# Performance work log

Hardware: AMD Instinct MI355X
Metric: run time of the kernel (lower is better)

## Reference

```python
import jax, jax.numpy as jnp
import numpy as np

EPS = 1e-05
BOUNDARY = 1.0 - EPS
LAMBDA_REP = 1.0


def poincare_dist_matrix(z):
    # z: [B, D]. Pairwise Poincare distance, same math as PoincareDistance.forward:
    #   squnorm = clamp(|u|^2, 0, boundary); sqdist = |u - v|^2 (unclamped)
    #   x = 2*sqdist/((1-squnorm)*(1-sqvnorm)) + 1; d = log(x + sqrt(x^2 - 1))
    sq = jnp.sum(z * z, axis=-1)                      # [B] raw squared norms
    squ = jnp.clip(sq, 0.0, BOUNDARY)                 # clamped norms (as in torch)
    # |u-v|^2 via norms + gram matrix (avoids materializing [B,B,D])
    sqdist = jnp.maximum(sq[:, None] + sq[None, :] - 2.0 * (z @ z.T), 0.0)  # [B,B]
    alpha = 1.0 - squ
    x = sqdist / (alpha[:, None] * alpha[None, :]) * 2.0 + 1.0
    # safe sqrt: diagonal has x==1 exactly; clamp mirrors torch backward's clamp(min=eps)
    t = jnp.sqrt(jnp.maximum(x * x - 1.0, EPS * EPS))
    return jnp.log(x + t)


def setup_inputs() -> dict:
    key = jax.random.key(0)
    k1, k2, k3, k4 = jax.random.split(key, 4)
    N, B, D = 8192, 4096, 16
    z = jax.random.normal(k1, (B, D), dtype=jnp.float32)
    # place embeddings strictly inside the Poincare ball (norm < 0.7)
    z = 0.7 * z / (1.0 + jnp.linalg.norm(z, axis=-1, keepdims=True))
    w_vals = jax.random.uniform(k2, (N, N), dtype=jnp.float32)
    keep = jax.random.uniform(k3, (N, N)) < 0.05
    W = jnp.where(keep, w_vals, 0.0)
    indices = jax.random.randint(k4, (B,), 0, N)
    return {"z": z, "W": W, "indices": indices}


def reference(z, W, indices):
    B = z.shape[0]
    W_batch = W[indices][:, indices]                  # [B,B] gathered weights
    eye = jnp.eye(B, dtype=bool)
    W_batch = jnp.where(eye, 0.0, W_batch)
    D_low = poincare_dist_matrix(z)                   # [B,B]
    non_neighbors = jnp.where(eye, 0.0, (W_batch == 0.0).astype(z.dtype))
    loss_attract = jnp.sum(W_batch * D_low) / (jnp.sum(W_batch) + 1e-08)
    loss_repel = jnp.sum(non_neighbors * jnp.exp(-D_low)) / (jnp.sum(non_neighbors) + 1e-08)
    return loss_attract + LAMBDA_REP * loss_repel
```

## Files before the change

### kernel.cpp

```cpp
#include <hip/hip_runtime.h>
#include <math.h>

#define TI 32
#define BLOCK 512
#define DIM 16
#define JC 256

typedef short bf16x8 __attribute__((ext_vector_type(8)));
typedef float f32x16 __attribute__((ext_vector_type(16)));

static __device__ __forceinline__ short f2bf(float f) {
    unsigned u = __builtin_bit_cast(unsigned, f);
    unsigned r = (u + 0x7FFFu + ((u >> 16) & 1u)) >> 16;
    return (short)r;
}

__global__ __launch_bounds__(1024) void sort_kernel(
    const int* __restrict__ idx, int B, int N,
    int* __restrict__ perm, int* __restrict__ skey)
{
    extern __shared__ int hist[];
    __shared__ int wsum[16];
    const int tid = threadIdx.x;
    const int lane = tid & 63, wid = tid >> 6;
    for (int b = tid; b < N; b += 1024) hist[b] = 0;
    __syncthreads();
    for (int j = tid; j < B; j += 1024) atomicAdd(&hist[idx[j]], 1);
    __syncthreads();
    const int PB = (N + 1023) >> 10;
    int local[8];
    int sum = 0;
    #pragma unroll
    for (int q = 0; q < 8; ++q) {
        if (q < PB) {
            int b = tid * PB + q;
            local[q] = sum;
            if (b < N) sum += hist[b];
        }
    }
    int v = sum;
    for (int off = 1; off < 64; off <<= 1) {
        int u = __shfl_up(v, off);
        if (lane >= off) v += u;
    }
    if (lane == 63) wsum[wid] = v;
    __syncthreads();
    if (tid < 16) {
        int t = wsum[tid];
        for (int off = 1; off < 16; off <<= 1) {
            int u = __shfl_up(t, off);
            if (lane >= off) t += u;
        }
        wsum[tid] = t;
    }
    __syncthreads();
    int base = (wid == 0) ? 0 : wsum[wid - 1];
    int excl = base + v - sum;
    #pragma unroll
    for (int q = 0; q < 8; ++q) {
        if (q < PB) {
            int b = tid * PB + q;
            if (b < N) hist[b] = excl + local[q];
        }
    }
    __syncthreads();
    for (int j = tid; j < B; j += 1024) {
        int k = idx[j];
        int pos = atomicAdd(&hist[k], 1);
        perm[pos] = j;
        skey[pos] = k;
    }
}

__global__ __launch_bounds__(256) void prep_kernel(
    const float* __restrict__ z, const int* __restrict__ perm, int B,
    float* __restrict__ zs, float* __restrict__ sqs, float* __restrict__ ras)
{
    int r = blockIdx.x * 256 + threadIdx.x;
    if (r >= B) return;
    int p = perm[r];
    const float4* src = reinterpret_cast<const float4*>(z + (size_t)p * DIM);
    float4* dst = reinterpret_cast<float4*>(zs + (size_t)r * DIM);
    float s = 0.f;
    #pragma unroll
    for (int q = 0; q < 4; ++q) {
        float4 v = src[q];
        dst[q] = v;
        s = fmaf(v.x, v.x, s); s = fmaf(v.y, v.y, s);
        s = fmaf(v.z, v.z, s); s = fmaf(v.w, v.w, s);
    }
    sqs[r] = s;
    float sc = fminf(fmaxf(s, 0.f), 0.99999f);
    ras[r] = 1.0f / (1.0f - sc);
}

__global__ __launch_bounds__(BLOCK, 4) void pair_kernel(
    const float* __restrict__ W, const int* __restrict__ skey,
    const float* __restrict__ zs, const float* __restrict__ sqs,
    const float* __restrict__ ras,
    int B, int N, double* __restrict__ partial)
{
    __shared__ double red[BLOCK / 64][4];

    const int tid  = threadIdx.x;
    const int wv   = tid >> 6;
    const int lane = tid & 63;
    const int half = lane >> 5;
    const int sub  = lane & 31;
    const int i0   = blockIdx.x * TI;
    const int jr0  = blockIdx.y * JC;

    const int irow  = i0 + sub;
    const int jrank = jr0 + wv * 32 + sub;
    const int kj    = skey[jrank];

    float wg[16];
    #pragma unroll
    for (int r = 0; r < 16; ++r) {
        const int rowm = (r & 3) + 8 * (r >> 2) + 4 * half;
        const int skr  = skey[i0 + rowm];
        wg[r] = W[(size_t)skr * (size_t)N + (size_t)kj];
    }

    const float ui = ras[irow],  vi = sqs[irow]  * ui;
    const float uj = ras[jrank], vj = sqs[jrank] * uj;
    bf16x8 a1, b1, a2, b2;
    {
        const float4* zp = reinterpret_cast<const float4*>(zs + (size_t)irow * DIM + 8 * half);
        float4 p0 = zp[0], p1 = zp[1];
        float s = 2.0f * ui;
        a1[0]=f2bf(s*p0.x); a1[1]=f2bf(s*p0.y); a1[2]=f2bf(s*p0.z); a1[3]=f2bf(s*p0.w);
        a1[4]=f2bf(s*p1.x); a1[5]=f2bf(s*p1.y); a1[6]=f2bf(s*p1.z); a1[7]=f2bf(s*p1.w);
    }
    {
        const float4* zp = reinterpret_cast<const float4*>(zs + (size_t)jrank * DIM + 8 * half);
        float4 p0 = zp[0], p1 = zp[1];
        float s = -2.0f * uj;
        b1[0]=f2bf(s*p0.x); b1[1]=f2bf(s*p0.y); b1[2]=f2bf(s*p0.z); b1[3]=f2bf(s*p0.w);
        b1[4]=f2bf(s*p1.x); b1[5]=f2bf(s*p1.y); b1[6]=f2bf(s*p1.z); b1[7]=f2bf(s*p1.w);
    }
    #pragma unroll
    for (int e = 0; e < 8; ++e) { a2[e] = 0; b2[e] = 0; }
    if (half == 0) {
        a2[0] = f2bf(2.0f * vi); a2[1] = f2bf(2.0f * ui);
        b2[0] = f2bf(uj);        b2[1] = f2bf(vj);
    }

    f32x16 acc = {};
    acc = __builtin_amdgcn_mfma_f32_32x32x16_bf16(a1, b1, acc, 0, 0, 0);
    acc = __builtin_amdgcn_mfma_f32_32x32x16_bf16(a2, b2, acc, 0, 0, 0);

    float a_wd = 0.f, a_w = 0.f, a_rep = 0.f, a_cnt = 0.f;
    #pragma unroll
    for (int r = 0; r < 16; ++r) {
        const int rowm = (r & 3) + 8 * (r >> 2) + 4 * half;
        float xm1 = fmaxf(acc[r], 0.0f);
        float w = wg[r];
        float t = __builtin_amdgcn_sqrtf(fmaxf(xm1 * (xm1 + 2.0f), 1e-10f));
        float x = xm1 + 1.0f;
        float d = __logf(x + t);
        bool diag = ((i0 + rowm) == jrank);
        if (diag) w = 0.0f;
        a_wd += w * d;
        a_w  += w;
        bool rep = (w == 0.0f) && !diag;
        a_rep += rep ? (x - t) : 0.0f;
        a_cnt += rep ? 1.0f : 0.0f;
    }

    double vals[4] = { (double)a_wd, (double)a_w, (double)a_rep, (double)a_cnt };
    #pragma unroll
    for (int c = 0; c < 4; ++c) {
        double v = vals[c];
        for (int off = 32; off > 0; off >>= 1) v += __shfl_down(v, off);
        vals[c] = v;
    }
    if (lane == 0) {
        #pragma unroll
        for (int c = 0; c < 4; ++c) red[wv][c] = vals[c];
    }
    __syncthreads();
    if (tid == 0) {
        double tot[4] = {0.0, 0.0, 0.0, 0.0};
        for (int wgt = 0; wgt < BLOCK / 64; ++wgt)
            for (int c = 0; c < 4; ++c) tot[c] += red[wgt][c];
        size_t bid = (size_t)blockIdx.y * gridDim.x + blockIdx.x;
        #pragma unroll
        for (int c = 0; c < 4; ++c) partial[bid * 4 + c] = tot[c];
    }
}

__global__ __launch_bounds__(1024) void finish_kernel(
    const double* __restrict__ partial, int nblocks, float* __restrict__ out)
{
    __shared__ double red[16][4];
    const int tid = threadIdx.x, wid = tid >> 6, lane = tid & 63;
    double vals[4] = {0.0, 0.0, 0.0, 0.0};
    for (int b = tid; b < nblocks; b += 1024)
        for (int c = 0; c < 4; ++c) vals[c] += partial[(size_t)b * 4 + c];
    #pragma unroll
    for (int c = 0; c < 4; ++c) {
        double v = vals[c];
        for (int off = 32; off > 0; off >>= 1) v += __shfl_down(v, off);
        vals[c] = v;
    }
    if (lane == 0)
        for (int c = 0; c < 4; ++c) red[wid][c] = vals[c];
    __syncthreads();
    if (tid == 0) {
        double tot[4] = {0.0, 0.0, 0.0, 0.0};
        for (int wgt = 0; wgt < 16; ++wgt)
            for (int c = 0; c < 4; ++c) tot[c] += red[wgt][c];
        double la = tot[0] / (tot[1] + 1e-8);
        double lr = tot[2] / (tot[3] + 1e-8);
        out[0] = (float)(la + lr);
    }
}

extern "C" void kernel_launch(void* const* d_in, const int* in_sizes, int n_in,
                              void* d_out, int out_size, void* d_ws, size_t ws_size,
                              hipStream_t stream)
{
    const float* z  = (const float*)d_in[0];
    const float* W  = (const float*)d_in[1];
    const int* idx  = (const int*)d_in[2];
    const int B = in_sizes[2];
    int N = 1;
    while ((long long)(N + 1) * (N + 1) <= (long long)in_sizes[1]) ++N;

    const int nblocks = (B / TI) * (B / JC);

    double* partial = (double*)d_ws;
    int* perm     = (int*)(partial + (size_t)nblocks * 4);
    int* skey     = perm + B;
    float* zs     = (float*)(skey + B);
    float* sqs    = zs + (size_t)B * DIM;
    float* ras    = sqs + B;

    sort_kernel<<<1, 1024, (size_t)N * sizeof(int), stream>>>(idx, B, N, perm, skey);
    prep_kernel<<<(B + 255) / 256, 256, 0, stream>>>(z, perm, B, zs, sqs, ras);

    dim3 grid(B / TI, B / JC);
    pair_kernel<<<grid, BLOCK, 0, stream>>>(W, skey, zs, sqs, ras, B, N, partial);
    finish_kernel<<<1, 1024, 0, stream>>>(partial, nblocks, (float*)d_out);
}
```

Baseline: 42.77 us.

## Fuse prep and finish kernels into pair kernel with atomic last-block reduction

```diff
diff --git a/kernel.cpp b/kernel.cpp
--- a/kernel.cpp
+++ b/kernel.cpp
@@ -72,33 +72,10 @@
     }
 }
 
-__global__ __launch_bounds__(256) void prep_kernel(
-    const float* __restrict__ z, const int* __restrict__ perm, int B,
-    float* __restrict__ zs, float* __restrict__ sqs, float* __restrict__ ras)
-{
-    int r = blockIdx.x * 256 + threadIdx.x;
-    if (r >= B) return;
-    int p = perm[r];
-    const float4* src = reinterpret_cast<const float4*>(z + (size_t)p * DIM);
-    float4* dst = reinterpret_cast<float4*>(zs + (size_t)r * DIM);
-    float s = 0.f;
-    #pragma unroll
-    for (int q = 0; q < 4; ++q) {
-        float4 v = src[q];
-        dst[q] = v;
-        s = fmaf(v.x, v.x, s); s = fmaf(v.y, v.y, s);
-        s = fmaf(v.z, v.z, s); s = fmaf(v.w, v.w, s);
-    }
-    sqs[r] = s;
-    float sc = fminf(fmaxf(s, 0.f), 0.99999f);
-    ras[r] = 1.0f / (1.0f - sc);
-}
-
 __global__ __launch_bounds__(BLOCK, 4) void pair_kernel(
     const float* __restrict__ W, const int* __restrict__ skey,
-    const float* __restrict__ zs, const float* __restrict__ sqs,
-    const float* __restrict__ ras,
-    int B, int N, double* __restrict__ partial)
+    const int* __restrict__ perm, const float* __restrict__ z,
+    int B, int N, int nblocks, double* __restrict__ ws, float* __restrict__ out)
 {
     __shared__ double red[BLOCK / 64][4];
 
@@ -122,22 +99,39 @@
         wg[r] = W[(size_t)skr * (size_t)N + (size_t)kj];
     }
 
-    const float ui = ras[irow],  vi = sqs[irow]  * ui;
-    const float uj = ras[jrank], vj = sqs[jrank] * uj;
+    float zi[DIM], zj[DIM];
+    {
+        const float4* zp = reinterpret_cast<const float4*>(z + (size_t)perm[irow] * DIM);
+        #pragma unroll
+        for (int q = 0; q < 4; ++q) {
+            float4 vv = zp[q];
+            zi[4*q+0]=vv.x; zi[4*q+1]=vv.y; zi[4*q+2]=vv.z; zi[4*q+3]=vv.w;
+        }
+    }
+    {
+        const float4* zp = reinterpret_cast<const float4*>(z + (size_t)perm[jrank] * DIM);
+        #pragma unroll
+        for (int q = 0; q < 4; ++q) {
+            float4 vv = zp[q];
+            zj[4*q+0]=vv.x; zj[4*q+1]=vv.y; zj[4*q+2]=vv.z; zj[4*q+3]=vv.w;
+        }
+    }
+    float sqi = 0.f, sqj = 0.f;
+    #pragma unroll
+    for (int k = 0; k < DIM; ++k) { sqi = fmaf(zi[k], zi[k], sqi); sqj = fmaf(zj[k], zj[k], sqj); }
+    const float ui = 1.0f / (1.0f - fminf(fmaxf(sqi, 0.f), 0.99999f)), vi = sqi * ui;
+    const float uj = 1.0f / (1.0f - fminf(fmaxf(sqj, 0.f), 0.99999f)), vj = sqj * uj;
+
     bf16x8 a1, b1, a2, b2;
     {
-        const float4* zp = reinterpret_cast<const float4*>(zs + (size_t)irow * DIM + 8 * half);
-        float4 p0 = zp[0], p1 = zp[1];
         float s = 2.0f * ui;
-        a1[0]=f2bf(s*p0.x); a1[1]=f2bf(s*p0.y); a1[2]=f2bf(s*p0.z); a1[3]=f2bf(s*p0.w);
-        a1[4]=f2bf(s*p1.x); a1[5]=f2bf(s*p1.y); a1[6]=f2bf(s*p1.z); a1[7]=f2bf(s*p1.w);
-    }
-    {
-        const float4* zp = reinterpret_cast<const float4*>(zs + (size_t)jrank * DIM + 8 * half);
-        float4 p0 = zp[0], p1 = zp[1];
+        #pragma unroll
+        for (int e = 0; e < 8; ++e) a1[e] = f2bf(s * zi[8 * half + e]);
+    }
+    {
         float s = -2.0f * uj;
-        b1[0]=f2bf(s*p0.x); b1[1]=f2bf(s*p0.y); b1[2]=f2bf(s*p0.z); b1[3]=f2bf(s*p0.w);
-        b1[4]=f2bf(s*p1.x); b1[5]=f2bf(s*p1.y); b1[6]=f2bf(s*p1.z); b1[7]=f2bf(s*p1.w);
+        #pragma unroll
+        for (int e = 0; e < 8; ++e) b1[e] = f2bf(s * zj[8 * half + e]);
     }
     #pragma unroll
     for (int e = 0; e < 8; ++e) { a2[e] = 0; b2[e] = 0; }
@@ -184,36 +178,17 @@
         double tot[4] = {0.0, 0.0, 0.0, 0.0};
         for (int wgt = 0; wgt < BLOCK / 64; ++wgt)
             for (int c = 0; c < 4; ++c) tot[c] += red[wgt][c];
-        size_t bid = (size_t)blockIdx.y * gridDim.x + blockIdx.x;
-        #pragma unroll
-        for (int c = 0; c < 4; ++c) partial[bid * 4 + c] = tot[c];
-    }
-}
-
-__global__ __launch_bounds__(1024) void finish_kernel(
-    const double* __restrict__ partial, int nblocks, float* __restrict__ out)
-{
-    __shared__ double red[16][4];
-    const int tid = threadIdx.x, wid = tid >> 6, lane = tid & 63;
-    double vals[4] = {0.0, 0.0, 0.0, 0.0};
-    for (int b = tid; b < nblocks; b += 1024)
-        for (int c = 0; c < 4; ++c) vals[c] += partial[(size_t)b * 4 + c];
-    #pragma unroll
-    for (int c = 0; c < 4; ++c) {
-        double v = vals[c];
-        for (int off = 32; off > 0; off >>= 1) v += __shfl_down(v, off);
-        vals[c] = v;
-    }
-    if (lane == 0)
-        for (int c = 0; c < 4; ++c) red[wid][c] = vals[c];
-    __syncthreads();
-    if (tid == 0) {
-        double tot[4] = {0.0, 0.0, 0.0, 0.0};
-        for (int wgt = 0; wgt < 16; ++wgt)
-            for (int c = 0; c < 4; ++c) tot[c] += red[wgt][c];
-        double la = tot[0] / (tot[1] + 1e-8);
-        double lr = tot[2] / (tot[3] + 1e-8);
-        out[0] = (float)(la + lr);
+        #pragma unroll
+        for (int c = 0; c < 4; ++c) atomicAdd(&ws[c], tot[c]);
+        __threadfence();
+        unsigned tk = atomicAdd((unsigned*)&ws[4], 1u);
+        if (tk == (unsigned)(nblocks - 1)) {
+            double s0 = atomicAdd(&ws[0], 0.0);
+            double s1 = atomicAdd(&ws[1], 0.0);
+            double s2 = atomicAdd(&ws[2], 0.0);
+            double s3 = atomicAdd(&ws[3], 0.0);
+            out[0] = (float)(s0 / (s1 + 1e-8) + s2 / (s3 + 1e-8));
+        }
     }
 }
 
@@ -230,17 +205,14 @@
 
     const int nblocks = (B / TI) * (B / JC);
 
-    double* partial = (double*)d_ws;
-    int* perm     = (int*)(partial + (size_t)nblocks * 4);
-    int* skey     = perm + B;
-    float* zs     = (float*)(skey + B);
-    float* sqs    = zs + (size_t)B * DIM;
-    float* ras    = sqs + B;
+    double* ws = (double*)d_ws;
+    int* perm = (int*)(ws + 6);
+    int* skey = perm + B;
+    hipMemsetAsync(ws, 0, 6 * sizeof(double), stream);
 
     sort_kernel<<<1, 1024, (size_t)N * sizeof(int), stream>>>(idx, B, N, perm, skey);
-    prep_kernel<<<(B + 255) / 256, 256, 0, stream>>>(z, perm, B, zs, sqs, ras);
 
     dim3 grid(B / TI, B / JC);
-    pair_kernel<<<grid, BLOCK, 0, stream>>>(W, skey, zs, sqs, ras, B, N, partial);
-    finish_kernel<<<1, 1024, 0, stream>>>(partial, nblocks, (float*)d_out);
-}
+    pair_kernel<<<grid, BLOCK, 0, stream>>>(W, skey, perm, z, B, N, nblocks,
+                                            ws, (float*)d_out);
+}
```

Result: slower. 166.9 us (+290.2%).

## Precompute bf16 operands and row offsets in prep, shrink pair-kernel loads and reductions

Applied to the files above, without the earlier changes.

```diff
diff --git a/kernel.cpp b/kernel.cpp
--- a/kernel.cpp
+++ b/kernel.cpp
@@ -17,7 +17,7 @@
 
 __global__ __launch_bounds__(1024) void sort_kernel(
     const int* __restrict__ idx, int B, int N,
-    int* __restrict__ perm, int* __restrict__ skey)
+    int* __restrict__ perm, int* __restrict__ skey, unsigned* __restrict__ skeyN)
 {
     extern __shared__ int hist[];
     __shared__ int wsum[16];
@@ -69,35 +69,53 @@
         int pos = atomicAdd(&hist[k], 1);
         perm[pos] = j;
         skey[pos] = k;
+        skeyN[pos] = (unsigned)k * (unsigned)N;
     }
 }
 
 __global__ __launch_bounds__(256) void prep_kernel(
     const float* __restrict__ z, const int* __restrict__ perm, int B,
-    float* __restrict__ zs, float* __restrict__ sqs, float* __restrict__ ras)
+    unsigned short* __restrict__ zb, unsigned* __restrict__ pka,
+    unsigned* __restrict__ pkb)
 {
     int r = blockIdx.x * 256 + threadIdx.x;
     if (r >= B) return;
     int p = perm[r];
     const float4* src = reinterpret_cast<const float4*>(z + (size_t)p * DIM);
-    float4* dst = reinterpret_cast<float4*>(zs + (size_t)r * DIM);
+    float zr[DIM];
     float s = 0.f;
     #pragma unroll
     for (int q = 0; q < 4; ++q) {
-        float4 v = src[q];
-        dst[q] = v;
-        s = fmaf(v.x, v.x, s); s = fmaf(v.y, v.y, s);
-        s = fmaf(v.z, v.z, s); s = fmaf(v.w, v.w, s);
-    }
-    sqs[r] = s;
+        float4 vv = src[q];
+        zr[4*q+0]=vv.x; zr[4*q+1]=vv.y; zr[4*q+2]=vv.z; zr[4*q+3]=vv.w;
+        s = fmaf(vv.x, vv.x, s); s = fmaf(vv.y, vv.y, s);
+        s = fmaf(vv.z, vv.z, s); s = fmaf(vv.w, vv.w, s);
+    }
     float sc = fminf(fmaxf(s, 0.f), 0.99999f);
-    ras[r] = 1.0f / (1.0f - sc);
+    float u = 1.0f / (1.0f - sc);
+    float v = s * u;
+    unsigned short h[DIM];
+    float sa = 2.0f * u;
+    #pragma unroll
+    for (int k = 0; k < DIM; ++k) h[k] = (unsigned short)f2bf(sa * zr[k]);
+    uint4* dst = reinterpret_cast<uint4*>(zb + (size_t)r * DIM);
+    uint4 w0, w1;
+    w0.x = h[0] | ((unsigned)h[1] << 16);  w0.y = h[2] | ((unsigned)h[3] << 16);
+    w0.z = h[4] | ((unsigned)h[5] << 16);  w0.w = h[6] | ((unsigned)h[7] << 16);
+    w1.x = h[8] | ((unsigned)h[9] << 16);  w1.y = h[10] | ((unsigned)h[11] << 16);
+    w1.z = h[12] | ((unsigned)h[13] << 16); w1.w = h[14] | ((unsigned)h[15] << 16);
+    dst[0] = w0; dst[1] = w1;
+    pka[r] = (unsigned)(unsigned short)f2bf(2.0f * v)
+           | ((unsigned)(unsigned short)f2bf(2.0f * u) << 16);
+    pkb[r] = (unsigned)(unsigned short)f2bf(u)
+           | ((unsigned)(unsigned short)f2bf(v) << 16);
 }
 
 __global__ __launch_bounds__(BLOCK, 4) void pair_kernel(
     const float* __restrict__ W, const int* __restrict__ skey,
-    const float* __restrict__ zs, const float* __restrict__ sqs,
-    const float* __restrict__ ras,
+    const unsigned* __restrict__ skeyN,
+    const unsigned short* __restrict__ zb,
+    const unsigned* __restrict__ pka, const unsigned* __restrict__ pkb,
     int B, int N, double* __restrict__ partial)
 {
     __shared__ double red[BLOCK / 64][4];
@@ -112,38 +130,27 @@
 
     const int irow  = i0 + sub;
     const int jrank = jr0 + wv * 32 + sub;
-    const int kj    = skey[jrank];
+    const unsigned kj = (unsigned)skey[jrank];
 
     float wg[16];
     #pragma unroll
     for (int r = 0; r < 16; ++r) {
         const int rowm = (r & 3) + 8 * (r >> 2) + 4 * half;
-        const int skr  = skey[i0 + rowm];
-        wg[r] = W[(size_t)skr * (size_t)N + (size_t)kj];
-    }
-
-    const float ui = ras[irow],  vi = sqs[irow]  * ui;
-    const float uj = ras[jrank], vj = sqs[jrank] * uj;
-    bf16x8 a1, b1, a2, b2;
-    {
-        const float4* zp = reinterpret_cast<const float4*>(zs + (size_t)irow * DIM + 8 * half);
-        float4 p0 = zp[0], p1 = zp[1];
-        float s = 2.0f * ui;
-        a1[0]=f2bf(s*p0.x); a1[1]=f2bf(s*p0.y); a1[2]=f2bf(s*p0.z); a1[3]=f2bf(s*p0.w);
-        a1[4]=f2bf(s*p1.x); a1[5]=f2bf(s*p1.y); a1[6]=f2bf(s*p1.z); a1[7]=f2bf(s*p1.w);
-    }
-    {
-        const float4* zp = reinterpret_cast<const float4*>(zs + (size_t)jrank * DIM + 8 * half);
-        float4 p0 = zp[0], p1 = zp[1];
-        float s = -2.0f * uj;
-        b1[0]=f2bf(s*p0.x); b1[1]=f2bf(s*p0.y); b1[2]=f2bf(s*p0.z); b1[3]=f2bf(s*p0.w);
-        b1[4]=f2bf(s*p1.x); b1[5]=f2bf(s*p1.y); b1[6]=f2bf(s*p1.z); b1[7]=f2bf(s*p1.w);
-    }
-    #pragma unroll
-    for (int e = 0; e < 8; ++e) { a2[e] = 0; b2[e] = 0; }
+        const unsigned off = skeyN[i0 + rowm] + kj;
+        wg[r] = W[(size_t)off];
+    }
+
+    bf16x8 a1 = *reinterpret_cast<const bf16x8*>(zb + (size_t)irow * DIM + 8 * half);
+    uint4 bv = *reinterpret_cast<const uint4*>(zb + (size_t)jrank * DIM + 8 * half);
+    bv.x ^= 0x80008000u; bv.y ^= 0x80008000u;
+    bv.z ^= 0x80008000u; bv.w ^= 0x80008000u;
+    bf16x8 b1 = __builtin_bit_cast(bf16x8, bv);
+
+    bf16x8 a2 = {}, b2 = {};
     if (half == 0) {
-        a2[0] = f2bf(2.0f * vi); a2[1] = f2bf(2.0f * ui);
-        b2[0] = f2bf(uj);        b2[1] = f2bf(vj);
+        unsigned pa = pka[irow], pb = pkb[jrank];
+        a2[0] = (short)(pa & 0xffffu); a2[1] = (short)(pa >> 16);
+        b2[0] = (short)(pb & 0xffffu); b2[1] = (short)(pb >> 16);
     }
 
     f32x16 acc = {};
@@ -168,16 +175,16 @@
         a_cnt += rep ? 1.0f : 0.0f;
     }
 
-    double vals[4] = { (double)a_wd, (double)a_w, (double)a_rep, (double)a_cnt };
+    float vals[4] = { a_wd, a_w, a_rep, a_cnt };
     #pragma unroll
     for (int c = 0; c < 4; ++c) {
-        double v = vals[c];
+        float v = vals[c];
         for (int off = 32; off > 0; off >>= 1) v += __shfl_down(v, off);
         vals[c] = v;
     }
     if (lane == 0) {
         #pragma unroll
-        for (int c = 0; c < 4; ++c) red[wv][c] = vals[c];
+        for (int c = 0; c < 4; ++c) red[wv][c] = (double)vals[c];
     }
     __syncthreads();
     if (tid == 0) {
@@ -231,16 +238,19 @@
     const int nblocks = (B / TI) * (B / JC);
 
     double* partial = (double*)d_ws;
-    int* perm     = (int*)(partial + (size_t)nblocks * 4);
-    int* skey     = perm + B;
-    float* zs     = (float*)(skey + B);
-    float* sqs    = zs + (size_t)B * DIM;
-    float* ras    = sqs + B;
-
-    sort_kernel<<<1, 1024, (size_t)N * sizeof(int), stream>>>(idx, B, N, perm, skey);
-    prep_kernel<<<(B + 255) / 256, 256, 0, stream>>>(z, perm, B, zs, sqs, ras);
+    int* perm       = (int*)(partial + (size_t)nblocks * 4);
+    int* skey       = perm + B;
+    unsigned* skeyN = (unsigned*)(skey + B);
+    unsigned* pka   = skeyN + B;
+    unsigned* pkb   = pka + B;
+    unsigned short* zbv = (unsigned short*)(pkb + B);
+
+    sort_kernel<<<1, 1024, (size_t)N * sizeof(int), stream>>>(
+        idx, B, N, perm, skey, skeyN);
+    prep_kernel<<<(B + 255) / 256, 256, 0, stream>>>(z, perm, B, zbv, pka, pkb);
 
     dim3 grid(B / TI, B / JC);
-    pair_kernel<<<grid, BLOCK, 0, stream>>>(W, skey, zs, sqs, ras, B, N, partial);
+    pair_kernel<<<grid, BLOCK, 0, stream>>>(W, skey, skeyN, zbv, pka, pkb,
+                                            B, N, partial);
     finish_kernel<<<1, 1024, 0, stream>>>(partial, nblocks, (float*)d_out);
 }
```

New measurement: 41.66 us. -2.6%, faster.
